# Kernel tuning notes

Measured on AMD Instinct MI355X. Metric: run time of the kernel, lower is better.

## Reference

```python
import jax, jax.numpy as jnp
import numpy as np

N, E, F, T, C, HOR = 50000, 800000, 4, 12, 32, 12


def setup_inputs() -> dict:
    key = jax.random.key(0)
    ks = jax.random.split(key, 24)
    def rn(k, shape, s=0.1):
        return jax.random.normal(k, shape, jnp.float32) * s
    inp = {
        "x": jax.random.normal(ks[0], (N, F, T), jnp.float32),
        "edge_index": jax.random.randint(ks[1], (2, E), 0, N, dtype=jnp.int64),
        "edge_weight": jax.random.uniform(ks[2], (E,), jnp.float32),
        "attention": jax.random.uniform(ks[3], (T,), jnp.float32),
    }
    names = ["Wz", "bz", "Wlz", "blz", "Wr", "br", "Wlr", "blr", "Wh", "bh", "Wlh", "blh"]
    shapes = [(F, C), (C,), (2 * C, C), (C,), (F, C), (C,), (2 * C, C), (C,), (F, C), (C,), (2 * C, C), (C,)]
    for i, (n, s) in enumerate(zip(names, shapes)):
        inp[n] = rn(ks[4 + i], s)
    inp["Wout"] = rn(ks[20], (C, HOR))
    inp["bout"] = jnp.zeros((HOR,), jnp.float32)
    return inp


def reference(x, edge_index, edge_weight, attention,
              Wz, bz, Wlz, blz, Wr, br, Wlr, blr, Wh, bh, Wlh, blh,
              Wout, bout):
    n = x.shape[0]
    c = Wz.shape[1]
    row, col = edge_index[0], edge_index[1]

    # GCN normalization with self-loops (weight 1): A_hat = D^-1/2 (A+I) D^-1/2
    deg = jax.ops.segment_sum(edge_weight, col, num_segments=n) + 1.0
    dis = 1.0 / jnp.sqrt(deg)                      # deg >= 1 thanks to self-loop
    norm = dis[row] * edge_weight * dis[col]       # [E]
    self_norm = dis * dis                          # [N] self-loop coefficient

    def conv(xt, W, b):
        # xt: [N, F] -> [N, C]; sparse normalized aggregation over edge list
        xw = xt @ W
        agg = jax.ops.segment_sum(norm[:, None] * xw[row], col, num_segments=n)
        return agg + self_norm[:, None] * xw + b

    probs = jax.nn.softmax(attention)              # attention over periods
    H0 = jnp.zeros((n, c), x.dtype)                # A3TGCN passes H=None each period
    H_accum = jnp.zeros((n, c), x.dtype)
    for t in range(x.shape[2]):                    # fixed small period loop (as original)
        xt = x[:, :, t]
        Z = jax.nn.sigmoid(jnp.concatenate([conv(xt, Wz, bz), H0], axis=1) @ Wlz + blz)
        R = jax.nn.sigmoid(jnp.concatenate([conv(xt, Wr, br), H0], axis=1) @ Wlr + blr)
        Ht = jnp.tanh(jnp.concatenate([conv(xt, Wh, bh), H0 * R], axis=1) @ Wlh + blh)
        Hn = Z * H0 + (1.0 - Z) * Ht               # GRU update from zero state
        H_accum = H_accum + probs[t] * Hn

    h = jax.nn.relu(H_accum)
    return h @ Wout + bout
```

## Files before the change

kernel.cpp:

```cpp
#include <hip/hip_runtime.h>
#include <hip/hip_bf16.h>

#define NN 50000
#define NE 800000
#define FD 4
#define TD 12
#define CD 32
#define HD 12
#define FT 48
#define NBANK 8

#define OFF_HEAD   0
#define OFF_PAY    400000
#define OFF_DIS    3600000
#define OFF_XS     3650000
#define OFF_CST    6050000

__global__ void build_pre_kernel(const int* __restrict__ ei, const float* __restrict__ w,
                                 int* __restrict__ head, int4* __restrict__ pay4,
                                 const float* __restrict__ Wz, const float* __restrict__ bz,
                                 const float* __restrict__ Wlz, const float* __restrict__ blz,
                                 const float* __restrict__ Wh, const float* __restrict__ bh,
                                 const float* __restrict__ Wlh, const float* __restrict__ blh,
                                 const float* __restrict__ attention,
                                 float* __restrict__ cst) {
    int tid = threadIdx.x;
    if (blockIdx.x < (NE / 256)) {
        int e = blockIdx.x * 256 + tid;
        int r = ei[e];
        int c = ei[NE + e];
        int old = atomicExch(&head[(e & (NBANK-1)) * NN + c], e);
        pay4[e] = make_int4(r, __float_as_int(w[e]), old, 0);
        return;
    }
    if (tid < 128) {
        int f = tid >> 5, c = tid & 31;
        float s = 0.f, s2 = 0.f;
        #pragma unroll
        for (int k = 0; k < 32; ++k) {
            s  += Wz[f*32 + k] * Wlz[k*32 + c];
            s2 += Wh[f*32 + k] * Wlh[k*32 + c];
        }
        cst[tid]       = s;
        cst[160 + tid] = s2;
    } else if (tid < 160) {
        int c = tid - 128;
        float s = blz[c], s2 = blh[c];
        #pragma unroll
        for (int k = 0; k < 32; ++k) {
            s  += bz[k] * Wlz[k*32 + c];
            s2 += bh[k] * Wlh[k*32 + c];
        }
        cst[128 + c] = s;
        cst[288 + c] = s2;
    } else if (tid == 160) {
        float m = -1e30f;
        for (int t = 0; t < TD; ++t) m = fmaxf(m, attention[t]);
        float e[TD], s = 0.f;
        #pragma unroll
        for (int t = 0; t < TD; ++t) { e[t] = __expf(attention[t] - m); s += e[t]; }
        float inv = 1.f / s;
        #pragma unroll
        for (int t = 0; t < TD; ++t) cst[320 + t] = e[t] * inv;
    }
}

__global__ void degdis_xs_kernel(const int* __restrict__ head, const int4* __restrict__ pay4,
                                 const float* __restrict__ x, float* __restrict__ dis,
                                 float* __restrict__ xs) {
    int t = blockIdx.x * blockDim.x + threadIdx.x;
    int i = t >> 4;
    int g = t & 15;
    float s = 0.f;
    if (g < 8) {
        int e = head[g * NN + i];
        while (e >= 0) {
            int4 p = pay4[e];
            s += __int_as_float(p.y);
            e = p.z;
        }
    }
    s += __shfl_xor(s, 1, 8);
    s += __shfl_xor(s, 2, 8);
    s += __shfl_xor(s, 4, 8);
    float dsum = __shfl(s, 0, 16);
    float di = rsqrtf(dsum + 1.0f);
    if (g == 0) dis[i] = di;
    const float3* x3 = (const float3*)x;
    float3 xv = x3[i * 16 + g];
    ((float3*)xs)[i * 16 + g] = make_float3(di * xv.x, di * xv.y, di * xv.z);
}

__global__ __launch_bounds__(256) void gather_gru_kernel(
        const float* __restrict__ xs, const float* __restrict__ dis,
        const int* __restrict__ head, const int4* __restrict__ pay4,
        const float* __restrict__ cst, const float* __restrict__ Wout,
        const float* __restrict__ bout, float* __restrict__ out) {
    __shared__ int2  smeta[16][64];
    __shared__ float sy[16][FT];
    __shared__ float hbuf[16][CD];
    __shared__ float sAz[128], sAh[128], sCz[32], sCh[32], sP[TD];
    __shared__ float sWout[CD * HD], sBout[HD];

    int tid = threadIdx.x;
    if (tid < 128) { sAz[tid] = cst[tid]; sAh[tid] = cst[160 + tid]; }
    if (tid < 32)  { sCz[tid] = cst[128 + tid]; sCh[tid] = cst[288 + tid]; }
    if (tid < TD)  { sP[tid] = cst[320 + tid]; sBout[tid] = bout[tid]; }
    for (int k = tid; k < CD * HD; k += 256) sWout[k] = Wout[k];
    __syncthreads();

    int g  = tid & 15;
    int ln = tid >> 4;
    int i  = blockIdx.x * 16 + ln;

    const float3* xs3 = (const float3*)xs;
    float d = dis[i];
    float3 a = xs3[i * 16 + g];
    float ax = a.x, ay = a.y, az = a.z;

    int e = (g < 8) ? head[g * NN + i] : -1;

    while (true) {
        int r0=0,r1=0,r2=0,r3=0,r4=0,r5=0,r6=0,r7=0;
        float n0=0,n1=0,n2=0,n3=0,n4=0,n5=0,n6=0,n7=0;
        int cnt = 0;
        #define STEP(RK,NK) if (e >= 0) { int4 p = pay4[e]; RK = p.x; \
            NK = __int_as_float(p.y); e = p.z; ++cnt; }
        STEP(r0,n0) STEP(r1,n1) STEP(r2,n2) STEP(r3,n3)
        STEP(r4,n4) STEP(r5,n5) STEP(r6,n6) STEP(r7,n7)
        #undef STEP

        int incl = cnt;
        #pragma unroll
        for (int dd = 1; dd < 8; dd <<= 1) {
            int t2 = __shfl_up(incl, dd, 16);
            if (g >= dd) incl += t2;
        }
        int S = __shfl(incl, 7, 16);
        if (S == 0) break;
        int off = incl - cnt;

        if (cnt > 0) smeta[ln][off + 0] = make_int2(r0, __float_as_int(n0));
        if (cnt > 1) smeta[ln][off + 1] = make_int2(r1, __float_as_int(n1));
        if (cnt > 2) smeta[ln][off + 2] = make_int2(r2, __float_as_int(n2));
        if (cnt > 3) smeta[ln][off + 3] = make_int2(r3, __float_as_int(n3));
        if (cnt > 4) smeta[ln][off + 4] = make_int2(r4, __float_as_int(n4));
        if (cnt > 5) smeta[ln][off + 5] = make_int2(r5, __float_as_int(n5));
        if (cnt > 6) smeta[ln][off + 6] = make_int2(r6, __float_as_int(n6));
        if (cnt > 7) smeta[ln][off + 7] = make_int2(r7, __float_as_int(n7));
        __builtin_amdgcn_wave_barrier();

        #pragma unroll 8
        for (int k = 0; k < S; ++k) {
            int2 m = smeta[ln][k];
            float nv = __int_as_float(m.y);
            float3 v = xs3[m.x * 16 + g];
            ax += nv * v.x; ay += nv * v.y; az += nv * v.z;
        }
    }

    sy[ln][g*3 + 0] = d * ax;
    sy[ln][g*3 + 1] = d * ay;
    sy[ln][g*3 + 2] = d * az;
    __syncthreads();

    {
        int c0 = g, c1 = g + 16;
        float az00 = sAz[c0], az01 = sAz[32+c0], az02 = sAz[64+c0], az03 = sAz[96+c0];
        float az10 = sAz[c1], az11 = sAz[32+c1], az12 = sAz[64+c1], az13 = sAz[96+c1];
        float ah00 = sAh[c0], ah01 = sAh[32+c0], ah02 = sAh[64+c0], ah03 = sAh[96+c0];
        float ah10 = sAh[c1], ah11 = sAh[32+c1], ah12 = sAh[64+c1], ah13 = sAh[96+c1];
        float cz0 = sCz[c0], cz1 = sCz[c1], ch0 = sCh[c0], ch1 = sCh[c1];

        float hacc0 = 0.f, hacc1 = 0.f;
        #pragma unroll
        for (int t = 0; t < TD; ++t) {
            float y0 = sy[ln][0*TD + t];
            float y1 = sy[ln][1*TD + t];
            float y2 = sy[ln][2*TD + t];
            float y3 = sy[ln][3*TD + t];
            float z0 = cz0 + y0*az00 + y1*az01 + y2*az02 + y3*az03;
            float z1 = cz1 + y0*az10 + y1*az11 + y2*az12 + y3*az13;
            float h0 = ch0 + y0*ah00 + y1*ah01 + y2*ah02 + y3*ah03;
            float h1 = ch1 + y0*ah10 + y1*ah11 + y2*ah12 + y3*ah13;
            float Z0 = 1.f / (1.f + __expf(-z0));
            float Z1 = 1.f / (1.f + __expf(-z1));
            float e0 = __expf(2.f * h0);
            float e1 = __expf(2.f * h1);
            float H0v = (e0 - 1.f) / (e0 + 1.f);
            float H1v = (e1 - 1.f) / (e1 + 1.f);
            float p = sP[t];
            hacc0 += p * (1.f - Z0) * H0v;
            hacc1 += p * (1.f - Z1) * H1v;
        }
        hbuf[ln][c0] = fmaxf(hacc0, 0.f);
        hbuf[ln][c1] = fmaxf(hacc1, 0.f);
    }
    __syncthreads();

    if (tid < 16 * HD) {
        int lnode = tid / HD, hor = tid - lnode * HD;
        int gn = blockIdx.x * 16 + lnode;
        float s = sBout[hor];
        #pragma unroll
        for (int k = 0; k < CD; ++k) s += hbuf[lnode][k] * sWout[k * HD + hor];
        out[gn * HD + hor] = s;
    }
}

extern "C" void kernel_launch(void* const* d_in, const int* in_sizes, int n_in,
                              void* d_out, int out_size, void* d_ws, size_t ws_size,
                              hipStream_t stream) {
    const float* x      = (const float*)d_in[0];
    const int*   ei     = (const int*)d_in[1];
    const float* ew     = (const float*)d_in[2];
    const float* attn   = (const float*)d_in[3];
    const float* Wz     = (const float*)d_in[4];
    const float* bz     = (const float*)d_in[5];
    const float* Wlz    = (const float*)d_in[6];
    const float* blz    = (const float*)d_in[7];
    const float* Wh     = (const float*)d_in[12];
    const float* bh     = (const float*)d_in[13];
    const float* Wlh    = (const float*)d_in[14];
    const float* blh    = (const float*)d_in[15];
    const float* Wout   = (const float*)d_in[16];
    const float* bout   = (const float*)d_in[17];
    float* out = (float*)d_out;

    float* ws   = (float*)d_ws;
    int*   head = (int*)(ws + OFF_HEAD);
    int4*  pay4 = (int4*)(ws + OFF_PAY);
    float* dis  = ws + OFF_DIS;
    float* xs   = ws + OFF_XS;
    float* cst  = ws + OFF_CST;

    hipMemsetAsync(head, 0xFF, NBANK * NN * sizeof(int), stream);

    build_pre_kernel<<<NE / 256 + 1, 256, 0, stream>>>(ei, ew, head, pay4,
                                                       Wz, bz, Wlz, blz,
                                                       Wh, bh, Wlh, blh, attn, cst);

    degdis_xs_kernel<<<NN * 16 / 256, 256, 0, stream>>>(head, pay4, x, dis, xs);

    gather_gru_kernel<<<NN / 16, 256, 0, stream>>>(
        xs, dis, head, pay4, cst, Wout, bout, out);
}
```

Before: 199.4 us.

## Fuse memset, build, degree and gather stages into one cooperative persistent kernel

Replaces the memset plus three kernel launches with a single cooperative kernel that uses grid-wide syncs between the head-reset, edge-list build, degree/scaling and gather-GRU phases. Blocks loop persistently over nodes and edges. It is meant to remove launch gaps and per-kernel tail effects. In exchange the gather phase runs with a capped grid (maxB*256, at most 2048 blocks), so there is less parallelism, and grid.sync adds its own overhead. The grid size is computed as occupancy-per-CU times 256 rather than times the CU count, which looks unintended. The old multi-kernel path stays as a fallback if the cooperative launch fails.

```diff
diff --git a/kernel.cpp b/kernel.cpp
--- a/kernel.cpp
+++ b/kernel.cpp
@@ -1,5 +1,8 @@
 #include <hip/hip_runtime.h>
+#include <hip/hip_cooperative_groups.h>
 #include <hip/hip_bf16.h>
+
+namespace cg = cooperative_groups;
 
 #define NN 50000
 #define NE 800000
@@ -9,12 +12,247 @@
 #define HD 12
 #define FT 48
 #define NBANK 8
+#define NVB (NN/16)
 
 #define OFF_HEAD   0
 #define OFF_PAY    400000
 #define OFF_DIS    3600000
 #define OFF_XS     3650000
 #define OFF_CST    6050000
+
+struct SMem {
+    int2  smeta[16][64];
+    float sy[16][FT];
+    float hbuf[16][CD];
+    float sAz[128], sAh[128], sCz[32], sCh[32], sP[TD];
+    float sWout[CD * HD], sBout[HD];
+};
+
+__device__ __forceinline__ void dev_cst(int tid,
+        const float* __restrict__ Wz, const float* __restrict__ bz,
+        const float* __restrict__ Wlz, const float* __restrict__ blz,
+        const float* __restrict__ Wh, const float* __restrict__ bh,
+        const float* __restrict__ Wlh, const float* __restrict__ blh,
+        const float* __restrict__ attention, float* __restrict__ cst) {
+    if (tid < 128) {
+        int f = tid >> 5, c = tid & 31;
+        float s = 0.f, s2 = 0.f;
+        #pragma unroll
+        for (int k = 0; k < 32; ++k) {
+            s  += Wz[f*32 + k] * Wlz[k*32 + c];
+            s2 += Wh[f*32 + k] * Wlh[k*32 + c];
+        }
+        cst[tid]       = s;
+        cst[160 + tid] = s2;
+    } else if (tid < 160) {
+        int c = tid - 128;
+        float s = blz[c], s2 = blh[c];
+        #pragma unroll
+        for (int k = 0; k < 32; ++k) {
+            s  += bz[k] * Wlz[k*32 + c];
+            s2 += bh[k] * Wlh[k*32 + c];
+        }
+        cst[128 + c] = s;
+        cst[288 + c] = s2;
+    } else if (tid == 160) {
+        float m = -1e30f;
+        for (int t = 0; t < TD; ++t) m = fmaxf(m, attention[t]);
+        float e[TD], s = 0.f;
+        #pragma unroll
+        for (int t = 0; t < TD; ++t) { e[t] = __expf(attention[t] - m); s += e[t]; }
+        float inv = 1.f / s;
+        #pragma unroll
+        for (int t = 0; t < TD; ++t) cst[320 + t] = e[t] * inv;
+    }
+}
+
+__device__ __forceinline__ void dev_build(int e, const int* __restrict__ ei,
+                                          const float* __restrict__ w,
+                                          int* __restrict__ head, int4* __restrict__ pay4) {
+    int r = ei[e];
+    int c = ei[NE + e];
+    int old = atomicExch(&head[(e & (NBANK-1)) * NN + c], e);
+    pay4[e] = make_int4(r, __float_as_int(w[e]), old, 0);
+}
+
+__device__ __forceinline__ void dev_degdis_xs(int t, const int* __restrict__ head,
+                                              const int4* __restrict__ pay4,
+                                              const float* __restrict__ x,
+                                              float* __restrict__ dis,
+                                              float* __restrict__ xs) {
+    int i = t >> 4;
+    int g = t & 15;
+    float s = 0.f;
+    if (g < 8) {
+        int e = head[g * NN + i];
+        while (e >= 0) {
+            int4 p = pay4[e];
+            s += __int_as_float(p.y);
+            e = p.z;
+        }
+    }
+    s += __shfl_xor(s, 1, 8);
+    s += __shfl_xor(s, 2, 8);
+    s += __shfl_xor(s, 4, 8);
+    float dsum = __shfl(s, 0, 16);
+    float di = rsqrtf(dsum + 1.0f);
+    if (g == 0) dis[i] = di;
+    const float3* x3 = (const float3*)x;
+    float3 xv = x3[i * 16 + g];
+    ((float3*)xs)[i * 16 + g] = make_float3(di * xv.x, di * xv.y, di * xv.z);
+}
+
+__device__ __forceinline__ void dev_loadsm(int tid, SMem& sm, const float* __restrict__ cst,
+                                           const float* __restrict__ Wout,
+                                           const float* __restrict__ bout) {
+    if (tid < 128) { sm.sAz[tid] = cst[tid]; sm.sAh[tid] = cst[160 + tid]; }
+    if (tid < 32)  { sm.sCz[tid] = cst[128 + tid]; sm.sCh[tid] = cst[288 + tid]; }
+    if (tid < TD)  { sm.sP[tid] = cst[320 + tid]; sm.sBout[tid] = bout[tid]; }
+    for (int k = tid; k < CD * HD; k += 256) sm.sWout[k] = Wout[k];
+}
+
+__device__ __forceinline__ void dev_gather_vb(int vb, int tid, SMem& sm,
+        const float* __restrict__ xs, const float* __restrict__ dis,
+        const int* __restrict__ head, const int4* __restrict__ pay4,
+        float* __restrict__ out) {
+    int lane = tid & 63;
+    int g  = tid & 15;
+    int ln = tid >> 4;
+    int i  = vb * 16 + ln;
+
+    const float3* xs3 = (const float3*)xs;
+    float d = dis[i];
+    float3 a = xs3[i * 16 + g];
+    float ax = a.x, ay = a.y, az = a.z;
+
+    int e = (g < 8) ? head[g * NN + i] : -1;
+    (void)lane;
+
+    while (true) {
+        int r0=0,r1=0,r2=0,r3=0,r4=0,r5=0,r6=0,r7=0;
+        float n0=0,n1=0,n2=0,n3=0,n4=0,n5=0,n6=0,n7=0;
+        int cnt = 0;
+        #define STEP(RK,NK) if (e >= 0) { int4 p = pay4[e]; RK = p.x; \
+            NK = __int_as_float(p.y); e = p.z; ++cnt; }
+        STEP(r0,n0) STEP(r1,n1) STEP(r2,n2) STEP(r3,n3)
+        STEP(r4,n4) STEP(r5,n5) STEP(r6,n6) STEP(r7,n7)
+        #undef STEP
+
+        int incl = cnt;
+        #pragma unroll
+        for (int dd = 1; dd < 8; dd <<= 1) {
+            int t2 = __shfl_up(incl, dd, 16);
+            if (g >= dd) incl += t2;
+        }
+        int S = __shfl(incl, 7, 16);
+        if (S == 0) break;
+        int off = incl - cnt;
+
+        if (cnt > 0) sm.smeta[ln][off + 0] = make_int2(r0, __float_as_int(n0));
+        if (cnt > 1) sm.smeta[ln][off + 1] = make_int2(r1, __float_as_int(n1));
+        if (cnt > 2) sm.smeta[ln][off + 2] = make_int2(r2, __float_as_int(n2));
+        if (cnt > 3) sm.smeta[ln][off + 3] = make_int2(r3, __float_as_int(n3));
+        if (cnt > 4) sm.smeta[ln][off + 4] = make_int2(r4, __float_as_int(n4));
+        if (cnt > 5) sm.smeta[ln][off + 5] = make_int2(r5, __float_as_int(n5));
+        if (cnt > 6) sm.smeta[ln][off + 6] = make_int2(r6, __float_as_int(n6));
+        if (cnt > 7) sm.smeta[ln][off + 7] = make_int2(r7, __float_as_int(n7));
+        __builtin_amdgcn_wave_barrier();
+
+        #pragma unroll 8
+        for (int k = 0; k < S; ++k) {
+            int2 m = sm.smeta[ln][k];
+            float nv = __int_as_float(m.y);
+            float3 v = xs3[m.x * 16 + g];
+            ax += nv * v.x; ay += nv * v.y; az += nv * v.z;
+        }
+    }
+
+    sm.sy[ln][g*3 + 0] = d * ax;
+    sm.sy[ln][g*3 + 1] = d * ay;
+    sm.sy[ln][g*3 + 2] = d * az;
+    __syncthreads();
+
+    {
+        int c0 = g, c1 = g + 16;
+        float az00 = sm.sAz[c0], az01 = sm.sAz[32+c0], az02 = sm.sAz[64+c0], az03 = sm.sAz[96+c0];
+        float az10 = sm.sAz[c1], az11 = sm.sAz[32+c1], az12 = sm.sAz[64+c1], az13 = sm.sAz[96+c1];
+        float ah00 = sm.sAh[c0], ah01 = sm.sAh[32+c0], ah02 = sm.sAh[64+c0], ah03 = sm.sAh[96+c0];
+        float ah10 = sm.sAh[c1], ah11 = sm.sAh[32+c1], ah12 = sm.sAh[64+c1], ah13 = sm.sAh[96+c1];
+        float cz0 = sm.sCz[c0], cz1 = sm.sCz[c1], ch0 = sm.sCh[c0], ch1 = sm.sCh[c1];
+
+        float hacc0 = 0.f, hacc1 = 0.f;
+        #pragma unroll
+        for (int t = 0; t < TD; ++t) {
+            float y0 = sm.sy[ln][0*TD + t];
+            float y1 = sm.sy[ln][1*TD + t];
+            float y2 = sm.sy[ln][2*TD + t];
+            float y3 = sm.sy[ln][3*TD + t];
+            float z0 = cz0 + y0*az00 + y1*az01 + y2*az02 + y3*az03;
+            float z1 = cz1 + y0*az10 + y1*az11 + y2*az12 + y3*az13;
+            float h0 = ch0 + y0*ah00 + y1*ah01 + y2*ah02 + y3*ah03;
+            float h1 = ch1 + y0*ah10 + y1*ah11 + y2*ah12 + y3*ah13;
+            float Z0 = 1.f / (1.f + __expf(-z0));
+            float Z1 = 1.f / (1.f + __expf(-z1));
+            float e0 = __expf(2.f * h0);
+            float e1 = __expf(2.f * h1);
+            float H0v = (e0 - 1.f) / (e0 + 1.f);
+            float H1v = (e1 - 1.f) / (e1 + 1.f);
+            float p = sm.sP[t];
+            hacc0 += p * (1.f - Z0) * H0v;
+            hacc1 += p * (1.f - Z1) * H1v;
+        }
+        sm.hbuf[ln][c0] = fmaxf(hacc0, 0.f);
+        sm.hbuf[ln][c1] = fmaxf(hacc1, 0.f);
+    }
+    __syncthreads();
+
+    if (tid < 16 * HD) {
+        int lnode = tid / HD, hor = tid - lnode * HD;
+        int gn = vb * 16 + lnode;
+        float s = sm.sBout[hor];
+        #pragma unroll
+        for (int k = 0; k < CD; ++k) s += sm.hbuf[lnode][k] * sm.sWout[k * HD + hor];
+        out[gn * HD + hor] = s;
+    }
+    __syncthreads();
+}
+
+__global__ __launch_bounds__(256) void fused_all(
+        const float* __restrict__ x, const int* __restrict__ ei,
+        const float* __restrict__ ew,
+        const float* __restrict__ Wz, const float* __restrict__ bz,
+        const float* __restrict__ Wlz, const float* __restrict__ blz,
+        const float* __restrict__ Wh, const float* __restrict__ bh,
+        const float* __restrict__ Wlh, const float* __restrict__ blh,
+        const float* __restrict__ attn,
+        const float* __restrict__ Wout, const float* __restrict__ bout,
+        int* __restrict__ head, int4* __restrict__ pay4,
+        float* __restrict__ dis, float* __restrict__ xs,
+        float* __restrict__ cst, float* __restrict__ out) {
+    cg::grid_group grid = cg::this_grid();
+    __shared__ SMem sm;
+    int tid   = threadIdx.x;
+    int gsize = gridDim.x * 256;
+    int gtid  = blockIdx.x * 256 + tid;
+
+    for (int j = gtid; j < NBANK * NN; j += gsize) head[j] = -1;
+    if (blockIdx.x == 0) dev_cst(tid, Wz, bz, Wlz, blz, Wh, bh, Wlh, blh, attn, cst);
+    __threadfence();
+    grid.sync();
+
+    for (int e = gtid; e < NE; e += gsize) dev_build(e, ei, ew, head, pay4);
+    __threadfence();
+    grid.sync();
+
+    for (int t = gtid; t < NN * 16; t += gsize) dev_degdis_xs(t, head, pay4, x, dis, xs);
+    __threadfence();
+    grid.sync();
+
+    dev_loadsm(tid, sm, cst, Wout, bout);
+    __syncthreads();
+    for (int vb = blockIdx.x; vb < NVB; vb += gridDim.x)
+        dev_gather_vb(vb, tid, sm, xs, dis, head, pay4, out);
+}
 
 __global__ void build_pre_kernel(const int* __restrict__ ei, const float* __restrict__ w,
                                  int* __restrict__ head, int4* __restrict__ pay4,
@@ -26,69 +264,16 @@
                                  float* __restrict__ cst) {
     int tid = threadIdx.x;
     if (blockIdx.x < (NE / 256)) {
-        int e = blockIdx.x * 256 + tid;
-        int r = ei[e];
-        int c = ei[NE + e];
-        int old = atomicExch(&head[(e & (NBANK-1)) * NN + c], e);
-        pay4[e] = make_int4(r, __float_as_int(w[e]), old, 0);
+        dev_build(blockIdx.x * 256 + tid, ei, w, head, pay4);
         return;
     }
-    if (tid < 128) {
-        int f = tid >> 5, c = tid & 31;
-        float s = 0.f, s2 = 0.f;
-        #pragma unroll
-        for (int k = 0; k < 32; ++k) {
-            s  += Wz[f*32 + k] * Wlz[k*32 + c];
-            s2 += Wh[f*32 + k] * Wlh[k*32 + c];
-        }
-        cst[tid]       = s;
-        cst[160 + tid] = s2;
-    } else if (tid < 160) {
-        int c = tid - 128;
-        float s = blz[c], s2 = blh[c];
-        #pragma unroll
-        for (int k = 0; k < 32; ++k) {
-            s  += bz[k] * Wlz[k*32 + c];
-            s2 += bh[k] * Wlh[k*32 + c];
-        }
-        cst[128 + c] = s;
-        cst[288 + c] = s2;
-    } else if (tid == 160) {
-        float m = -1e30f;
-        for (int t = 0; t < TD; ++t) m = fmaxf(m, attention[t]);
-        float e[TD], s = 0.f;
-        #pragma unroll
-        for (int t = 0; t < TD; ++t) { e[t] = __expf(attention[t] - m); s += e[t]; }
-        float inv = 1.f / s;
-        #pragma unroll
-        for (int t = 0; t < TD; ++t) cst[320 + t] = e[t] * inv;
-    }
+    dev_cst(tid, Wz, bz, Wlz, blz, Wh, bh, Wlh, blh, attention, cst);
 }
 
 __global__ void degdis_xs_kernel(const int* __restrict__ head, const int4* __restrict__ pay4,
                                  const float* __restrict__ x, float* __restrict__ dis,
                                  float* __restrict__ xs) {
-    int t = blockIdx.x * blockDim.x + threadIdx.x;
-    int i = t >> 4;
-    int g = t & 15;
-    float s = 0.f;
-    if (g < 8) {
-        int e = head[g * NN + i];
-        while (e >= 0) {
-            int4 p = pay4[e];
-            s += __int_as_float(p.y);
-            e = p.z;
-        }
-    }
-    s += __shfl_xor(s, 1, 8);
-    s += __shfl_xor(s, 2, 8);
-    s += __shfl_xor(s, 4, 8);
-    float dsum = __shfl(s, 0, 16);
-    float di = rsqrtf(dsum + 1.0f);
-    if (g == 0) dis[i] = di;
-    const float3* x3 = (const float3*)x;
-    float3 xv = x3[i * 16 + g];
-    ((float3*)xs)[i * 16 + g] = make_float3(di * xv.x, di * xv.y, di * xv.z);
+    dev_degdis_xs(blockIdx.x * blockDim.x + threadIdx.x, head, pay4, x, dis, xs);
 }
 
 __global__ __launch_bounds__(256) void gather_gru_kernel(
@@ -96,116 +281,11 @@
         const int* __restrict__ head, const int4* __restrict__ pay4,
         const float* __restrict__ cst, const float* __restrict__ Wout,
         const float* __restrict__ bout, float* __restrict__ out) {
-    __shared__ int2  smeta[16][64];
-    __shared__ float sy[16][FT];
-    __shared__ float hbuf[16][CD];
-    __shared__ float sAz[128], sAh[128], sCz[32], sCh[32], sP[TD];
-    __shared__ float sWout[CD * HD], sBout[HD];
-
+    __shared__ SMem sm;
     int tid = threadIdx.x;
-    if (tid < 128) { sAz[tid] = cst[tid]; sAh[tid] = cst[160 + tid]; }
-    if (tid < 32)  { sCz[tid] = cst[128 + tid]; sCh[tid] = cst[288 + tid]; }
-    if (tid < TD)  { sP[tid] = cst[320 + tid]; sBout[tid] = bout[tid]; }
-    for (int k = tid; k < CD * HD; k += 256) sWout[k] = Wout[k];
-    __syncthreads();
-
-    int g  = tid & 15;
-    int ln = tid >> 4;
-    int i  = blockIdx.x * 16 + ln;
-
-    const float3* xs3 = (const float3*)xs;
-    float d = dis[i];
-    float3 a = xs3[i * 16 + g];
-    float ax = a.x, ay = a.y, az = a.z;
-
-    int e = (g < 8) ? head[g * NN + i] : -1;
-
-    while (true) {
-        int r0=0,r1=0,r2=0,r3=0,r4=0,r5=0,r6=0,r7=0;
-        float n0=0,n1=0,n2=0,n3=0,n4=0,n5=0,n6=0,n7=0;
-        int cnt = 0;
-        #define STEP(RK,NK) if (e >= 0) { int4 p = pay4[e]; RK = p.x; \
-            NK = __int_as_float(p.y); e = p.z; ++cnt; }
-        STEP(r0,n0) STEP(r1,n1) STEP(r2,n2) STEP(r3,n3)
-        STEP(r4,n4) STEP(r5,n5) STEP(r6,n6) STEP(r7,n7)
-        #undef STEP
-
-        int incl = cnt;
-        #pragma unroll
-        for (int dd = 1; dd < 8; dd <<= 1) {
-            int t2 = __shfl_up(incl, dd, 16);
-            if (g >= dd) incl += t2;
-        }
-        int S = __shfl(incl, 7, 16);
-        if (S == 0) break;
-        int off = incl - cnt;
-
-        if (cnt > 0) smeta[ln][off + 0] = make_int2(r0, __float_as_int(n0));
-        if (cnt > 1) smeta[ln][off + 1] = make_int2(r1, __float_as_int(n1));
-        if (cnt > 2) smeta[ln][off + 2] = make_int2(r2, __float_as_int(n2));
-        if (cnt > 3) smeta[ln][off + 3] = make_int2(r3, __float_as_int(n3));
-        if (cnt > 4) smeta[ln][off + 4] = make_int2(r4, __float_as_int(n4));
-        if (cnt > 5) smeta[ln][off + 5] = make_int2(r5, __float_as_int(n5));
-        if (cnt > 6) smeta[ln][off + 6] = make_int2(r6, __float_as_int(n6));
-        if (cnt > 7) smeta[ln][off + 7] = make_int2(r7, __float_as_int(n7));
-        __builtin_amdgcn_wave_barrier();
-
-        #pragma unroll 8
-        for (int k = 0; k < S; ++k) {
-            int2 m = smeta[ln][k];
-            float nv = __int_as_float(m.y);
-            float3 v = xs3[m.x * 16 + g];
-            ax += nv * v.x; ay += nv * v.y; az += nv * v.z;
-        }
-    }
-
-    sy[ln][g*3 + 0] = d * ax;
-    sy[ln][g*3 + 1] = d * ay;
-    sy[ln][g*3 + 2] = d * az;
-    __syncthreads();
-
-    {
-        int c0 = g, c1 = g + 16;
-        float az00 = sAz[c0], az01 = sAz[32+c0], az02 = sAz[64+c0], az03 = sAz[96+c0];
-        float az10 = sAz[c1], az11 = sAz[32+c1], az12 = sAz[64+c1], az13 = sAz[96+c1];
-        float ah00 = sAh[c0], ah01 = sAh[32+c0], ah02 = sAh[64+c0], ah03 = sAh[96+c0];
-        float ah10 = sAh[c1], ah11 = sAh[32+c1], ah12 = sAh[64+c1], ah13 = sAh[96+c1];
-        float cz0 = sCz[c0], cz1 = sCz[c1], ch0 = sCh[c0], ch1 = sCh[c1];
-
-        float hacc0 = 0.f, hacc1 = 0.f;
-        #pragma unroll
-        for (int t = 0; t < TD; ++t) {
-            float y0 = sy[ln][0*TD + t];
-            float y1 = sy[ln][1*TD + t];
-            float y2 = sy[ln][2*TD + t];
-            float y3 = sy[ln][3*TD + t];
-            float z0 = cz0 + y0*az00 + y1*az01 + y2*az02 + y3*az03;
-            float z1 = cz1 + y0*az10 + y1*az11 + y2*az12 + y3*az13;
-            float h0 = ch0 + y0*ah00 + y1*ah01 + y2*ah02 + y3*ah03;
-            float h1 = ch1 + y0*ah10 + y1*ah11 + y2*ah12 + y3*ah13;
-            float Z0 = 1.f / (1.f + __expf(-z0));
-            float Z1 = 1.f / (1.f + __expf(-z1));
-            float e0 = __expf(2.f * h0);
-            float e1 = __expf(2.f * h1);
-            float H0v = (e0 - 1.f) / (e0 + 1.f);
-            float H1v = (e1 - 1.f) / (e1 + 1.f);
-            float p = sP[t];
-            hacc0 += p * (1.f - Z0) * H0v;
-            hacc1 += p * (1.f - Z1) * H1v;
-        }
-        hbuf[ln][c0] = fmaxf(hacc0, 0.f);
-        hbuf[ln][c1] = fmaxf(hacc1, 0.f);
-    }
-    __syncthreads();
-
-    if (tid < 16 * HD) {
-        int lnode = tid / HD, hor = tid - lnode * HD;
-        int gn = blockIdx.x * 16 + lnode;
-        float s = sBout[hor];
-        #pragma unroll
-        for (int k = 0; k < CD; ++k) s += hbuf[lnode][k] * sWout[k * HD + hor];
-        out[gn * HD + hor] = s;
-    }
+    dev_loadsm(tid, sm, cst, Wout, bout);
+    __syncthreads();
+    dev_gather_vb(blockIdx.x, tid, sm, xs, dis, head, pay4, out);
 }
 
 extern "C" void kernel_launch(void* const* d_in, const int* in_sizes, int n_in,
@@ -234,14 +314,31 @@
     float* xs   = ws + OFF_XS;
     float* cst  = ws + OFF_CST;
 
-    hipMemsetAsync(head, 0xFF, NBANK * NN * sizeof(int), stream);
-
-    build_pre_kernel<<<NE / 256 + 1, 256, 0, stream>>>(ei, ew, head, pay4,
-                                                       Wz, bz, Wlz, blz,
-                                                       Wh, bh, Wlh, blh, attn, cst);
-
-    degdis_xs_kernel<<<NN * 16 / 256, 256, 0, stream>>>(head, pay4, x, dis, xs);
-
-    gather_gru_kernel<<<NN / 16, 256, 0, stream>>>(
-        xs, dis, head, pay4, cst, Wout, bout, out);
-}
+    bool coop_ok = false;
+    int maxB = 0;
+    if (hipOccupancyMaxActiveBlocksPerMultiprocessor(&maxB, fused_all, 256, 0) == hipSuccess
+        && maxB > 0) {
+        int grid = maxB * 256;
+        if (grid > 2048) grid = 2048;
+        void* args[] = { (void*)&x, (void*)&ei, (void*)&ew,
+                         (void*)&Wz, (void*)&bz, (void*)&Wlz, (void*)&blz,
+                         (void*)&Wh, (void*)&bh, (void*)&Wlh, (void*)&blh,
+                         (void*)&attn, (void*)&Wout, (void*)&bout,
+                         (void*)&head, (void*)&pay4, (void*)&dis, (void*)&xs,
+                         (void*)&cst, (void*)&out };
+        hipError_t err = hipLaunchCooperativeKernel(fused_all, dim3(grid), dim3(256),
+                                                    args, 0, stream);
+        if (err == hipSuccess) coop_ok = true;
+        else (void)hipGetLastError();
+    }
+
+    if (!coop_ok) {
+        hipMemsetAsync(head, 0xFF, NBANK * NN * sizeof(int), stream);
+        build_pre_kernel<<<NE / 256 + 1, 256, 0, stream>>>(ei, ew, head, pay4,
+                                                           Wz, bz, Wlz, blz,
+                                                           Wh, bh, Wlh, blh, attn, cst);
+        degdis_xs_kernel<<<NN * 16 / 256, 256, 0, stream>>>(head, pay4, x, dis, xs);
+        gather_gru_kernel<<<NVB, 256, 0, stream>>>(xs, dis, head, pay4, cst,
+                                                   Wout, bout, out);
+    }
+}
```

Result: slower. 524.3 us (+162.9%).
